# Performance work log

Measured on AMD Instinct MI355X. Metric: run time of the kernel, lower is better.

## Reference

```python
import jax, jax.numpy as jnp
import numpy as np
from math import gcd

N_SIG = 2097152   # signal length
L_FILT = 129      # FIR taps


def setup_inputs() -> dict:
    key = jax.random.key(0)
    k1, k2 = jax.random.split(key)
    x = jax.random.normal(k1, (N_SIG,), dtype=jnp.float32)
    h = jax.random.normal(k2, (L_FILT,), dtype=jnp.float32)
    return {"x": x, "h": h, "up": 3, "down": 2}


def _get_start_index(length):
    if length <= 2:
        return 0
    return (length - 1) // 2


def reference(x, h, up, down):
    # Reduce rates by gcd, as in the torch module.
    g = gcd(up, down)
    up, down = up // g, down // g
    if up == 1 and down == 1:
        return x
    N = x.shape[0]
    L = h.shape[0]
    # zero-stuff: x_up[::up] = up * x  (gain `up` matches resample_poly)
    x_up = jnp.zeros(up * N, dtype=x.dtype).at[::up].set(up * x)
    # full FIR convolution, then phase-offset strided downsample
    full = jnp.convolve(x_up, h.astype(x.dtype), mode="full")  # [up*N + L - 1]
    start = _get_start_index(L)
    n_out = -(-(N * up) // down)  # ceil(N*up/down)
    return full[start::down][:n_out]
```

## Files before the change

### kernel.cpp

```cpp
#include <hip/hip_runtime.h>


#define N_SIG   2097152
#define L_FILT  129
#define NTAPS   43
#define G       8
#define BLK     256
#define GROUPS_PER_BLK (BLK * G)
#define TILE_Q  4160
#define TILE_P  (TILE_Q + (TILE_Q / 16) * 4)

__global__ __launch_bounds__(BLK) void poly_kernel(
    const float* __restrict__ x, const float* __restrict__ h,
    float* __restrict__ out, int n_out)
{
    __shared__ float xs[TILE_P];
    __shared__ float hs[L_FILT];

    const int tid = threadIdx.x;
    const int b   = blockIdx.x;

    if (tid < L_FILT) hs[tid] = 3.0f * h[tid];

    const int tb = 4096 * b - 24;

    for (int q4 = tid; q4 < TILE_Q / 4; q4 += BLK) {
        const int gx = tb + 4 * q4;
        float4 v;
        if (gx >= 0 && gx + 3 < N_SIG) {
            v = *(const float4*)(x + gx);
        } else {
            v.x = (gx     >= 0 && gx     < N_SIG) ? x[gx]     : 0.0f;
            v.y = (gx + 1 >= 0 && gx + 1 < N_SIG) ? x[gx + 1] : 0.0f;
            v.z = (gx + 2 >= 0 && gx + 2 < N_SIG) ? x[gx + 2] : 0.0f;
            v.w = (gx + 3 >= 0 && gx + 3 < N_SIG) ? x[gx + 3] : 0.0f;
        }
        const int p = 4 * q4 + 4 * (q4 >> 2);
        *(float4*)(xs + p) = v;
    }
    __syncthreads();

    float w[64];
#pragma unroll
    for (int k = 0; k < 16; ++k) {
        const int p = 20 * tid + 4 * k + 4 * (k >> 2);
        const float4 v = *(const float4*)(xs + p);
        w[4 * k + 0] = v.x; w[4 * k + 1] = v.y;
        w[4 * k + 2] = v.z; w[4 * k + 3] = v.w;
    }

    float acc[3 * G];
#pragma unroll
    for (int k = 0; k < 3 * G; ++k) acc[k] = 0.0f;

#pragma unroll
    for (int i = 0; i < NTAPS; ++i) {
        const float h0 = hs[3 * i + 0];
        const float h1 = hs[3 * i + 1];
        const float h2 = hs[3 * i + 2];
#pragma unroll
        for (int g = 0; g < G; ++g) {
            const float xa = w[45 + 2 * g - i];
            const float xb = w[46 + 2 * g - i];
            acc[3 * g + 0] += xa * h1;
            acc[3 * g + 1] += xb * h0;
            acc[3 * g + 2] += xb * h2;
        }
    }

    const long ob = (long)GROUPS_PER_BLK * b * 3 + (long)(3 * G) * tid;
#pragma unroll
    for (int k = 0; k < 6; ++k) {
        if (ob + 4 * k + 3 < (long)n_out) {
            *(float4*)(out + ob + 4 * k) =
                make_float4(acc[4 * k + 0], acc[4 * k + 1],
                            acc[4 * k + 2], acc[4 * k + 3]);
        }
    }
}

extern "C" void kernel_launch(void* const* d_in, const int* in_sizes, int n_in,
                              void* d_out, int out_size, void* d_ws, size_t ws_size,
                              hipStream_t stream) {
    const float* x = (const float*)d_in[0];
    const float* h = (const float*)d_in[1];
    float* out = (float*)d_out;
    const int blocks = (out_size + 3 * GROUPS_PER_BLK - 1) / (3 * GROUPS_PER_BLK);
    poly_kernel<<<blocks, BLK, 0, stream>>>(x, h, out, out_size);
}
```

Baseline: 83.86 us.

## Shrink per-thread work, stream sliding windows from LDS, read taps directly from global

Restructures the polyphase kernel so each thread computes 2 output groups (6 outputs) instead of 8, with 128-thread blocks and a small 560-float tile. Instead of one 64-register window, the thread reloads overlapping 12-float windows from shared memory in software-pipelined chunks of 8 taps. Filter taps are now read straight from global memory as uniform loads, and the gain of 3 is applied at the end. Interior blocks skip bounds checks. This cuts register pressure and raises occupancy and block count, at the cost of more redundant shared-memory reads and halo overhead per output.

```diff
diff --git a/kernel.cpp b/kernel.cpp
--- a/kernel.cpp
+++ b/kernel.cpp
@@ -3,80 +3,123 @@
 
 #define N_SIG   2097152
 #define L_FILT  129
-#define NTAPS   43
-#define G       8
-#define BLK     256
-#define GROUPS_PER_BLK (BLK * G)
-#define TILE_Q  4160
-#define TILE_P  (TILE_Q + (TILE_Q / 16) * 4)
+#define G       2
+#define BLK     128
+#define GPB     (BLK * G)
+#define OPB     (3 * GPB)
+#define TILE_Q  560
 
-__global__ __launch_bounds__(BLK) void poly_kernel(
-    const float* __restrict__ x, const float* __restrict__ h,
-    float* __restrict__ out, int n_out)
-{
-    __shared__ float xs[TILE_P];
-    __shared__ float hs[L_FILT];
+template <int I0>
+__device__ __forceinline__ void load_win8(const float* __restrict__ xs, int tid,
+                                          float (&wz)[12]) {
+    const float4* p = (const float4*)(xs + 4 * tid + (40 - I0));
+    const float4 a = p[0], b = p[1], c = p[2];
+    wz[0] = a.x; wz[1]  = a.y; wz[2]  = a.z; wz[3]  = a.w;
+    wz[4] = b.x; wz[5]  = b.y; wz[6]  = b.z; wz[7]  = b.w;
+    wz[8] = c.x; wz[9]  = c.y; wz[10] = c.z; wz[11] = c.w;
+}
 
-    const int tid = threadIdx.x;
-    const int b   = blockIdx.x;
-
-    if (tid < L_FILT) hs[tid] = 3.0f * h[tid];
-
-    const int tb = 4096 * b - 24;
-
-    for (int q4 = tid; q4 < TILE_Q / 4; q4 += BLK) {
-        const int gx = tb + 4 * q4;
-        float4 v;
-        if (gx >= 0 && gx + 3 < N_SIG) {
-            v = *(const float4*)(x + gx);
-        } else {
-            v.x = (gx     >= 0 && gx     < N_SIG) ? x[gx]     : 0.0f;
-            v.y = (gx + 1 >= 0 && gx + 1 < N_SIG) ? x[gx + 1] : 0.0f;
-            v.z = (gx + 2 >= 0 && gx + 2 < N_SIG) ? x[gx + 2] : 0.0f;
-            v.w = (gx + 3 >= 0 && gx + 3 < N_SIG) ? x[gx + 3] : 0.0f;
-        }
-        const int p = 4 * q4 + 4 * (q4 >> 2);
-        *(float4*)(xs + p) = v;
-    }
-    __syncthreads();
-
-    float w[64];
+template <int I0>
+__device__ __forceinline__ void fma8(const float* __restrict__ h,
+                                     const float (&wz)[12], float (&acc)[6]) {
 #pragma unroll
-    for (int k = 0; k < 16; ++k) {
-        const int p = 20 * tid + 4 * k + 4 * (k >> 2);
-        const float4 v = *(const float4*)(xs + p);
-        w[4 * k + 0] = v.x; w[4 * k + 1] = v.y;
-        w[4 * k + 2] = v.z; w[4 * k + 3] = v.w;
-    }
-
-    float acc[3 * G];
+    for (int u = 0; u < 8; ++u) {
+        const float h0 = h[3 * (I0 + u) + 0];
+        const float h1 = h[3 * (I0 + u) + 1];
+        const float h2 = h[3 * (I0 + u) + 2];
 #pragma unroll
-    for (int k = 0; k < 3 * G; ++k) acc[k] = 0.0f;
-
-#pragma unroll
-    for (int i = 0; i < NTAPS; ++i) {
-        const float h0 = hs[3 * i + 0];
-        const float h1 = hs[3 * i + 1];
-        const float h2 = hs[3 * i + 2];
-#pragma unroll
-        for (int g = 0; g < G; ++g) {
-            const float xa = w[45 + 2 * g - i];
-            const float xb = w[46 + 2 * g - i];
+        for (int g = 0; g < 2; ++g) {
+            const float xa = wz[7 - u + 2 * g];
+            const float xb = wz[8 - u + 2 * g];
             acc[3 * g + 0] += xa * h1;
             acc[3 * g + 1] += xb * h0;
             acc[3 * g + 2] += xb * h2;
         }
     }
+}
 
-    const long ob = (long)GROUPS_PER_BLK * b * 3 + (long)(3 * G) * tid;
+__device__ __forceinline__ void load_tail(const float* __restrict__ xs, int tid,
+                                          float (&wt)[8]) {
+    const float4* p = (const float4*)(xs + 4 * tid + 4);
+    const float4 a = p[0], b = p[1];
+    wt[0] = a.x; wt[1] = a.y; wt[2] = a.z; wt[3] = a.w;
+    wt[4] = b.x; wt[5] = b.y; wt[6] = b.z; wt[7] = b.w;
+}
+
+__device__ __forceinline__ void fma_tail(const float* __restrict__ h,
+                                         const float (&wt)[8], float (&acc)[6]) {
 #pragma unroll
-    for (int k = 0; k < 6; ++k) {
-        if (ob + 4 * k + 3 < (long)n_out) {
-            *(float4*)(out + ob + 4 * k) =
-                make_float4(acc[4 * k + 0], acc[4 * k + 1],
-                            acc[4 * k + 2], acc[4 * k + 3]);
+    for (int u = 0; u < 3; ++u) {
+        const float h0 = h[3 * (40 + u) + 0];
+        const float h1 = h[3 * (40 + u) + 1];
+        const float h2 = h[3 * (40 + u) + 2];
+#pragma unroll
+        for (int g = 0; g < 2; ++g) {
+            const float xa = wt[3 - u + 2 * g];
+            const float xb = wt[4 - u + 2 * g];
+            acc[3 * g + 0] += xa * h1;
+            acc[3 * g + 1] += xb * h0;
+            acc[3 * g + 2] += xb * h2;
         }
     }
+}
+
+__global__ __launch_bounds__(BLK, 6) void poly_kernel(
+    const float* __restrict__ x, const float* __restrict__ h,
+    float* __restrict__ out, int nblocks)
+{
+    __shared__ alignas(16) float xs[TILE_Q];
+
+    const int tid = threadIdx.x;
+    const int b   = blockIdx.x;
+    const int tb  = 512 * b - 26;
+
+    if (b != 0 && b != nblocks - 1) {
+        {
+            const float* g0 = x + (tb + 4 * tid);
+            const float2 lo = *(const float2*)(g0);
+            const float2 hi = *(const float2*)(g0 + 2);
+            *(float4*)(xs + 4 * tid) = make_float4(lo.x, lo.y, hi.x, hi.y);
+        }
+        if (tid < TILE_Q / 4 - BLK) {
+            const float* g0 = x + (tb + 4 * (BLK + tid));
+            const float2 lo = *(const float2*)(g0);
+            const float2 hi = *(const float2*)(g0 + 2);
+            *(float4*)(xs + 4 * (BLK + tid)) = make_float4(lo.x, lo.y, hi.x, hi.y);
+        }
+    } else {
+        for (int q4 = tid; q4 < TILE_Q / 4; q4 += BLK) {
+            const int gx = tb + 4 * q4;
+            float4 v;
+            v.x = (gx     >= 0 && gx     < N_SIG) ? x[gx]     : 0.0f;
+            v.y = (gx + 1 >= 0 && gx + 1 < N_SIG) ? x[gx + 1] : 0.0f;
+            v.z = (gx + 2 >= 0 && gx + 2 < N_SIG) ? x[gx + 2] : 0.0f;
+            v.w = (gx + 3 >= 0 && gx + 3 < N_SIG) ? x[gx + 3] : 0.0f;
+            *(float4*)(xs + 4 * q4) = v;
+        }
+    }
+    __syncthreads();
+
+    float acc[6] = {0.f, 0.f, 0.f, 0.f, 0.f, 0.f};
+
+    float wA[12], wB[12], wC[12], wT[8];
+    load_win8<0>(xs, tid, wA);
+    load_win8<8>(xs, tid, wB);
+    load_win8<16>(xs, tid, wC);
+    fma8<0>(h, wA, acc);
+    load_win8<24>(xs, tid, wA);
+    fma8<8>(h, wB, acc);
+    load_win8<32>(xs, tid, wB);
+    fma8<16>(h, wC, acc);
+    load_tail(xs, tid, wT);
+    fma8<24>(h, wA, acc);
+    fma8<32>(h, wB, acc);
+    fma_tail(h, wT, acc);
+
+    const int ob = OPB * b + 6 * tid;
+    *(float2*)(out + ob + 0) = make_float2(3.0f * acc[0], 3.0f * acc[1]);
+    *(float2*)(out + ob + 2) = make_float2(3.0f * acc[2], 3.0f * acc[3]);
+    *(float2*)(out + ob + 4) = make_float2(3.0f * acc[4], 3.0f * acc[5]);
 }
 
 extern "C" void kernel_launch(void* const* d_in, const int* in_sizes, int n_in,
@@ -85,6 +128,6 @@
     const float* x = (const float*)d_in[0];
     const float* h = (const float*)d_in[1];
     float* out = (float*)d_out;
-    const int blocks = (out_size + 3 * GROUPS_PER_BLK - 1) / (3 * GROUPS_PER_BLK);
-    poly_kernel<<<blocks, BLK, 0, stream>>>(x, h, out, out_size);
+    const int blocks = (out_size + OPB - 1) / OPB;
+    poly_kernel<<<blocks, BLK, 0, stream>>>(x, h, out, blocks);
 }
```

Result: faster. 73.39 us (-12.5%).
